# Optimization experiments

Measured on AMD Instinct MI355X. Metric: run time of the kernel, lower is better.

## Reference

```python
import jax, jax.numpy as jnp
import numpy as np

B, N, K = 2, 8192, 16          # batch, points, ED_nsample
SA_C, DG_C = 128, 1024         # SA_conv_out, DG_conv_out
CAT_C = SA_C + SA_C // 4 + 4   # 164 channels into head


def _conv1(W, b, x):
    # 1x1 Conv1d: W [out,in], x [B,in,N]
    return jnp.einsum('oc,bcn->bon', W, x) + b[None, :, None]


def _bn_relu(x, g, be):
    # BatchNorm1d (training-mode batch stats) + ReLU, x [B,C,N]
    m = x.mean(axis=(0, 2), keepdims=True)
    v = x.var(axis=(0, 2), keepdims=True)
    return jax.nn.relu((x - m) * jax.lax.rsqrt(v + 1e-5) * g[None, :, None] + be[None, :, None])


def setup_inputs() -> dict:
    key = jax.random.key(0)
    ks = jax.random.split(key, 32)
    w = lambda k, s: jax.random.normal(k, s, jnp.float32) * 0.05
    p = {}
    p['pointcloud'] = jax.random.normal(ks[0], (B, N, 3), jnp.float32)
    p['h1'] = jax.random.normal(ks[1], (B, SA_C, N), jnp.float32)
    p['h2'] = jax.random.normal(ks[2], (B, DG_C, N), jnp.float32)
    p['numpoints'] = N
    # DG head convs 1024->256->64->32
    p['DG_w1'], p['DG_b1'] = w(ks[3], (256, DG_C)), jnp.zeros(256, jnp.float32)
    p['DG_g1'], p['DG_be1'] = jnp.ones(256, jnp.float32), jnp.zeros(256, jnp.float32)
    p['DG_w2'], p['DG_b2'] = w(ks[4], (64, 256)), jnp.zeros(64, jnp.float32)
    p['DG_g2'], p['DG_be2'] = jnp.ones(64, jnp.float32), jnp.zeros(64, jnp.float32)
    p['DG_w3'], p['DG_b3'] = w(ks[5], (SA_C // 4, 64)), jnp.zeros(SA_C // 4, jnp.float32)
    p['DG_g3'], p['DG_be3'] = jnp.ones(SA_C // 4, jnp.float32), jnp.zeros(SA_C // 4, jnp.float32)
    # ED MLP 3->4->4
    p['ED_w1'], p['ED_b1'] = w(ks[6], (3, 4)), jnp.zeros(4, jnp.float32)
    p['ED_w2'], p['ED_b2'] = w(ks[7], (4, 4)), jnp.zeros(4, jnp.float32)
    # head convs 164->512->256->128
    p['C_w1'], p['C_b1'] = w(ks[8], (512, CAT_C)), jnp.zeros(512, jnp.float32)
    p['C_g1'], p['C_be1'] = jnp.ones(512, jnp.float32), jnp.zeros(512, jnp.float32)
    p['C_w2'], p['C_b2'] = w(ks[9], (256, 512)), jnp.zeros(256, jnp.float32)
    p['C_g2'], p['C_be2'] = jnp.ones(256, jnp.float32), jnp.zeros(256, jnp.float32)
    p['C_w3'], p['C_b3'] = w(ks[10], (128, 256)), jnp.zeros(128, jnp.float32)
    p['C_g3'], p['C_be3'] = jnp.ones(128, jnp.float32), jnp.zeros(128, jnp.float32)
    return p


def reference(pointcloud, h1, h2, numpoints,
              DG_w1, DG_b1, DG_g1, DG_be1, DG_w2, DG_b2, DG_g2, DG_be2,
              DG_w3, DG_b3, DG_g3, DG_be3,
              ED_w1, ED_b1, ED_w2, ED_b2,
              C_w1, C_b1, C_g1, C_be1, C_w2, C_b2, C_g2, C_be2,
              C_w3, C_b3, C_g3, C_be3):
    xyz = pointcloud[..., :3]
    # DG branch head
    h2p = _bn_relu(_conv1(DG_w1, DG_b1, h2), DG_g1, DG_be1)
    h2p = _bn_relu(_conv1(DG_w2, DG_b2, h2p), DG_g2, DG_be2)
    h2p = _bn_relu(_conv1(DG_w3, DG_b3, h2p), DG_g3, DG_be3)
    # ED branch: brute-force knn on squared distances
    sq = jnp.sum(xyz * xyz, axis=-1)                               # [B,N]
    d = sq[:, :, None] + sq[:, None, :] - 2.0 * jnp.einsum('bnd,bmd->bnm', xyz, xyz)
    _, idx = jax.lax.top_k(-d, K)                                  # [B,N,K]
    nbr = jax.vmap(lambda pts, i: pts[i])(xyz, idx)                # [B,N,K,3]
    c = nbr - nbr.mean(axis=2, keepdims=True)
    cov = jnp.einsum('bnkd,bnke->bnde', c, c) / K                  # [B,N,3,3]
    ev = jnp.linalg.eigvalsh(cov)                                  # [B,N,3] ascending
    h3 = jax.nn.relu(ev @ ED_w1 + ED_b1) @ ED_w2 + ED_b2           # [B,N,4]
    # fuse and head
    z = jnp.concatenate([h1, h2p, jnp.transpose(h3, (0, 2, 1))], axis=1)
    z = _bn_relu(_conv1(C_w1, C_b1, z), C_g1, C_be1)
    z = _bn_relu(_conv1(C_w2, C_b2, z), C_g2, C_be2)
    z = _bn_relu(_conv1(C_w3, C_b3, z), C_g3, C_be3)
    return xyz, z
```

## Files before the change

kernel.cpp:

```cpp
#include <hip/hip_runtime.h>

#define NPTS 8192
#define BATCH 2

typedef __attribute__((ext_vector_type(8))) __bf16 bf16x8;
typedef __attribute__((ext_vector_type(4))) float f32x4;
typedef unsigned int u32;

__device__ inline unsigned short f2bf(float x) {
    unsigned u = __float_as_uint(x);
    u += 0x7fffu + ((u >> 16) & 1u);
    return (unsigned short)(u >> 16);
}
__device__ inline unsigned pack32(float d, unsigned idx) {
    unsigned u = __float_as_uint(d);
    u ^= ((unsigned)((int)u >> 31)) | 0x80000000u;
    return (u & 0xFFFFE000u) | idx;
}
__device__ inline unsigned bitonic64u(unsigned key, int lane) {
#pragma unroll
    for (int k = 2; k <= 64; k <<= 1) {
#pragma unroll
        for (int j = k >> 1; j > 0; j >>= 1) {
            unsigned o = __shfl_xor(key, j, 64);
            bool tmin = (((lane & k) == 0) == ((lane & j) == 0));
            key = ((o < key) == tmin) ? o : key;
        }
    }
    return key;
}
__device__ inline void ins16(unsigned& key, unsigned c, int lane) {
    unsigned prev = __shfl_up(key, 1, 64);
    if (lane == 0) prev = 0u;
    unsigned mx = prev > c ? prev : c;
    key = mx < key ? mx : key;
}
__device__ inline float distf(float4 q, float4 p) {
    return fmaf(-2.f, fmaf(q.z, p.z, fmaf(q.y, p.y, q.x * p.x)), q.w + p.w);
}

__global__ __launch_bounds__(256) void prep_presplit(
    const float* __restrict__ pc, float* __restrict__ oxyz, float4* __restrict__ pq,
    const float* __restrict__ W0, const float* __restrict__ W1,
    const float* __restrict__ W2, const float* __restrict__ W3,
    const float* __restrict__ W4, const float* __restrict__ W5,
    unsigned short* __restrict__ wsp) {
    int bx = blockIdx.x, tid = threadIdx.x;
    if (bx < 64) {
        int t = bx * 256 + tid;
        float x = pc[t * 3 + 0], y = pc[t * 3 + 1], z = pc[t * 3 + 2];
        oxyz[t * 3 + 0] = x; oxyz[t * 3 + 1] = y; oxyz[t * 3 + 2] = z;
        pq[t] = make_float4(x, y, z, fmaf(z, z, fmaf(y, y, x * x)));
        return;
    }
    int pb = bx - 64;
    const float* W; int O, C, OP; size_t off; int base;
    if (pb < 1024)      { W = W0; O = 256; C = 1024; OP = 256; off = 0;       base = 0; }
    else if (pb < 1152) { W = W1; O =  64; C =  256; OP = 128; off = 524288;  base = 1024; }
    else if (pb < 1184) { W = W2; O =  32; C =   64; OP = 128; off = 589824;  base = 1152; }
    else if (pb < 1568) { W = W3; O = 512; C =  164; OP = 512; off = 606208;  base = 1184; }
    else if (pb < 2080) { W = W4; O = 256; C =  512; OP = 256; off = 802816;  base = 1568; }
    else                { W = W5; O = 128; C =  256; OP = 128; off = 1064960; base = 2080; }
    unsigned short* dst = wsp + off;
    int t = (pb - base) * 256 + tid;
    int kk = t & 31;
    int o = (t >> 5) % OP;
    int kt = t / (OP * 32);
    int c = kt * 32 + kk;
    float x = (o < O && c < C) ? W[o * C + c] : 0.f;
    unsigned short hb = f2bf(x);
    float hf = __uint_as_float((unsigned)hb << 16);
    unsigned short lb = f2bf(x - hf);
    int s = kk >> 3, pos = kk & 7;
    int sst = s ^ ((o >> 1) & 3);
    dst[((size_t)(kt * 2) * OP + o) * 32 + sst * 8 + pos] = hb;
    dst[((size_t)(kt * 2 + 1) * OP + o) * 32 + sst * 8 + pos] = lb;
}

template <int MODE>
__device__ __forceinline__ void gemm_body(
    int nblk, int oy, int b,
    const unsigned short* __restrict__ Wsp, const float* __restrict__ bias,
    const float* __restrict__ X, float* __restrict__ out,
    int O, int C, int OP, int nK,
    const float2* __restrict__ stats,
    const float* __restrict__ h1, const float* __restrict__ h3,
    const float2* __restrict__ stats3,
    float2* __restrict__ partout) {
    const int N = NPTS;
    int tid = threadIdx.x;
    int lane = tid & 63, w = tid >> 6;
    int wm = w >> 1, wn = w & 1;
    int n0 = nblk * 64, o0 = oy * 64;
    int n = n0 + lane;

    __shared__ __align__(16) unsigned char lds[18432];
    __shared__ float ps1[2][64], ps2[2][64];
    unsigned char* WHp = lds;
    unsigned char* WLp = lds + 4096;
    unsigned char* XHp = lds + 8192;
    unsigned char* XLp = lds + 13312;

    f32x4 acc[2][2];
#pragma unroll
    for (int i = 0; i < 2; ++i)
#pragma unroll
        for (int j = 0; j < 2; ++j) acc[i][j] = (f32x4){0.f, 0.f, 0.f, 0.f};

    float xcur[8], xnxt[8];
    auto loadx = [&](int kt, float (&dst)[8]) {
#pragma unroll
        for (int i = 0; i < 8; ++i) {
            int c = kt * 32 + w * 8 + i;
            float x = 0.f;
            if (MODE == 0 || MODE == 1) {
                if (c < C) x = X[((size_t)(b * C + c)) * N + n];
            } else {
                if (c < 128)       x = h1[((size_t)(b * 128 + c)) * N + n];
                else if (c < 160)  x = X[((size_t)(b * 32 + (c - 128))) * N + n];
                else if (c < 164)  x = h3[((size_t)(b * 4 + (c - 160))) * N + n];
            }
            dst[i] = x;
        }
    };

    loadx(0, xcur);
    for (int kt = 0; kt < nK; ++kt) {
        int c0 = kt * 32;
#pragma unroll
        for (int comp = 0; comp < 2; ++comp) {
            const unsigned short* gb = Wsp + ((size_t)(kt * 2 + comp) * OP + o0) * 32;
            unsigned char* lb = comp ? WLp : WHp;
            __builtin_amdgcn_global_load_lds(
                (const __attribute__((address_space(1))) u32*)(gb + w * 512 + lane * 8),
                (__attribute__((address_space(3))) u32*)(lb + w * 1024),
                16, 0, 0);
        }
        {
            union { bf16x8 s; unsigned short u[8]; } hh, ll;
#pragma unroll
            for (int i = 0; i < 8; ++i) {
                int c = c0 + w * 8 + i;
                float x = xcur[i];
                if (MODE == 1) {
                    if (c < C) {
                        float2 st = stats[c];
                        x = fmaxf(fmaf(x, st.x, st.y), 0.f);
                    }
                } else if (MODE == 2) {
                    if (c >= 128 && c < 160) {
                        float2 st = stats3[c - 128];
                        x = fmaxf(fmaf(x, st.x, st.y), 0.f);
                    }
                }
                unsigned short hb = f2bf(x);
                float hf = __uint_as_float((unsigned)hb << 16);
                unsigned short lb = f2bf(x - hf);
                hh.u[i] = hb; ll.u[i] = lb;
            }
            *(bf16x8*)(XHp + lane * 80 + w * 16) = hh.s;
            *(bf16x8*)(XLp + lane * 80 + w * 16) = ll.s;
        }
        if (kt + 1 < nK) loadx(kt + 1, xnxt);
        __syncthreads();
        {
            int koff = (lane >> 4) * 16;
            bf16x8 bh[2], bl[2];
#pragma unroll
            for (int ni = 0; ni < 2; ++ni) {
                int rb = wn * 32 + ni * 16 + (lane & 15);
                bh[ni] = *(const bf16x8*)(XHp + rb * 80 + koff);
                bl[ni] = *(const bf16x8*)(XLp + rb * 80 + koff);
            }
#pragma unroll
            for (int mi = 0; mi < 2; ++mi) {
                int ra = wm * 32 + mi * 16 + (lane & 15);
                int sw = koff ^ ((((unsigned)ra >> 1) & 3) * 16);
                bf16x8 ah = *(const bf16x8*)(WHp + ra * 64 + sw);
                bf16x8 al = *(const bf16x8*)(WLp + ra * 64 + sw);
#pragma unroll
                for (int ni = 0; ni < 2; ++ni) {
                    acc[mi][ni] = __builtin_amdgcn_mfma_f32_16x16x32_bf16(ah, bh[ni], acc[mi][ni], 0, 0, 0);
                    acc[mi][ni] = __builtin_amdgcn_mfma_f32_16x16x32_bf16(ah, bl[ni], acc[mi][ni], 0, 0, 0);
                    acc[mi][ni] = __builtin_amdgcn_mfma_f32_16x16x32_bf16(al, bh[ni], acc[mi][ni], 0, 0, 0);
                }
            }
        }
        __syncthreads();
        if (kt + 1 < nK) {
#pragma unroll
            for (int i = 0; i < 8; ++i) xcur[i] = xnxt[i];
        }
    }
    int col = lane & 15, rq = lane >> 4;
#pragma unroll
    for (int mi = 0; mi < 2; ++mi) {
#pragma unroll
        for (int j = 0; j < 4; ++j) {
            int oloc = wm * 32 + mi * 16 + rq * 4 + j;
            int o = o0 + oloc;
            float s1 = 0.f, s2 = 0.f;
            if (o < O) {
                float bs = bias[o];
                float v0 = acc[mi][0][j] + bs;
                float v1 = acc[mi][1][j] + bs;
                float* po = out + ((size_t)(b * O + o)) * N + n0 + wn * 32 + col;
                po[0] = v0; po[16] = v1;
                s1 = v0 + v1;
                s2 = fmaf(v0, v0, v1 * v1);
            }
#pragma unroll
            for (int mm = 1; mm < 16; mm <<= 1) {
                s1 += __shfl_xor(s1, mm, 64);
                s2 += __shfl_xor(s2, mm, 64);
            }
            if (col == 0) { ps1[wn][oloc] = s1; ps2[wn][oloc] = s2; }
        }
    }
    __syncthreads();
    if (tid < 64) {
        int o = o0 + tid;
        if (o < O)
            partout[(size_t)o * 256 + b * 128 + nblk] =
                make_float2(ps1[0][tid] + ps1[1][tid], ps2[0][tid] + ps2[1][tid]);
    }
}

template <int MODE>
__global__ __launch_bounds__(256, 4) void mfma_gemm(
    const unsigned short* __restrict__ Wsp, const float* __restrict__ bias,
    const float* __restrict__ X, float* __restrict__ out,
    int O, int C, int OP, int nK,
    const float2* __restrict__ stats,
    const float* __restrict__ h1, const float* __restrict__ h3,
    const float2* __restrict__ stats3,
    float2* __restrict__ partout) {
    gemm_body<MODE>(blockIdx.x, blockIdx.y, blockIdx.z, Wsp, bias, X, out, O, C, OP, nK,
                    stats, h1, h3, stats3, partout);
}

__device__ void knn_body(int kb, const float4* __restrict__ pq,
                         const float* __restrict__ ew1, const float* __restrict__ eb1,
                         const float* __restrict__ ew2, const float* __restrict__ eb2,
                         float* __restrict__ h3) {
    int wv = threadIdx.x >> 6;
    int lane = threadIdx.x & 63;
    int sg = kb * 4 + wv;
    int b = sg >> 12;
    int iloc = (sg & 4095) << 1;
    const float4* pqb = pq + (size_t)b * NPTS;
    float4 Q0 = pqb[iloc + 0], Q1 = pqb[iloc + 1];

    float4 p = pqb[lane];
    unsigned k0 = bitonic64u(pack32(distf(Q0, p), lane), lane);
    unsigned k1 = bitonic64u(pack32(distf(Q1, p), lane), lane);
    unsigned tk0 = (unsigned)__builtin_amdgcn_readlane((int)k0, 15);
    unsigned tk1 = (unsigned)__builtin_amdgcn_readlane((int)k1, 15);

    float4 A = pqb[64 + lane];
    float4 B = pqb[128 + lane];
    for (int it = 1; it + 1 < 128; it += 2) {
        int tbA = it * 64, tbB = tbA + 64;
        int t3 = (it + 3 < 128) ? it + 3 : 0;
        float4 Cx = pqb[(it + 2) * 64 + lane];
        float4 Dx = pqb[t3 * 64 + lane];
        unsigned cA0 = pack32(distf(Q0, A), tbA + lane);
        unsigned cA1 = pack32(distf(Q1, A), tbA + lane);
        unsigned cB0 = pack32(distf(Q0, B), tbB + lane);
        unsigned cB1 = pack32(distf(Q1, B), tbB + lane);
        unsigned long long mA0 = __ballot(cA0 < tk0), mB0 = __ballot(cB0 < tk0);
        unsigned long long mA1 = __ballot(cA1 < tk1), mB1 = __ballot(cB1 < tk1);
        if (mA0 | mA1 | mB0 | mB1) {
            while (mA0) {
                int L = __ffsll((long long)mA0) - 1; mA0 &= mA0 - 1;
                ins16(k0, (unsigned)__builtin_amdgcn_readlane((int)cA0, L), lane);
            }
            while (mB0) {
                int L = __ffsll((long long)mB0) - 1; mB0 &= mB0 - 1;
                ins16(k0, (unsigned)__builtin_amdgcn_readlane((int)cB0, L), lane);
            }
            while (mA1) {
                int L = __ffsll((long long)mA1) - 1; mA1 &= mA1 - 1;
                ins16(k1, (unsigned)__builtin_amdgcn_readlane((int)cA1, L), lane);
            }
            while (mB1) {
                int L = __ffsll((long long)mB1) - 1; mB1 &= mB1 - 1;
                ins16(k1, (unsigned)__builtin_amdgcn_readlane((int)cB1, L), lane);
            }
            tk0 = (unsigned)__builtin_amdgcn_readlane((int)k0, 15);
            tk1 = (unsigned)__builtin_amdgcn_readlane((int)k1, 15);
        }
        A = Cx; B = Dx;
    }
    {
        int tbA = 127 * 64;
        unsigned cA0 = pack32(distf(Q0, A), tbA + lane);
        unsigned cA1 = pack32(distf(Q1, A), tbA + lane);
        unsigned long long mA0 = __ballot(cA0 < tk0);
        unsigned long long mA1 = __ballot(cA1 < tk1);
        while (mA0) {
            int L = __ffsll((long long)mA0) - 1; mA0 &= mA0 - 1;
            ins16(k0, (unsigned)__builtin_amdgcn_readlane((int)cA0, L), lane);
        }
        while (mA1) {
            int L = __ffsll((long long)mA1) - 1; mA1 &= mA1 - 1;
            ins16(k1, (unsigned)__builtin_amdgcn_readlane((int)cA1, L), lane);
        }
    }

    int g = lane >> 4, r = lane & 15;
    unsigned j0 = ((unsigned)__shfl((int)k0, r, 64)) & 8191u;
    unsigned j1 = ((unsigned)__shfl((int)k1, r, 64)) & 8191u;
    unsigned nj = ((g & 1) == 0) ? j0 : j1;

    float4 nb = pqb[nj];
    float sx = nb.x, sy = nb.y, sz = nb.z;
#pragma unroll
    for (int m = 1; m < 16; m <<= 1) {
        sx += __shfl_xor(sx, m, 64);
        sy += __shfl_xor(sy, m, 64);
        sz += __shfl_xor(sz, m, 64);
    }
    const float i16 = 1.f / 16.f;
    float cx = nb.x - sx * i16, cy = nb.y - sy * i16, cz = nb.z - sz * i16;
    float xx = cx * cx, xy = cx * cy, xz = cx * cz, yy = cy * cy, yz = cy * cz, zz = cz * cz;
#pragma unroll
    for (int m = 1; m < 16; m <<= 1) {
        xx += __shfl_xor(xx, m, 64); xy += __shfl_xor(xy, m, 64); xz += __shfl_xor(xz, m, 64);
        yy += __shfl_xor(yy, m, 64); yz += __shfl_xor(yz, m, 64); zz += __shfl_xor(zz, m, 64);
    }
    float a11 = xx * i16, a12 = xy * i16, a13 = xz * i16,
          a22 = yy * i16, a23 = yz * i16, a33 = zz * i16;
    float q = (a11 + a22 + a33) * (1.f / 3.f);
    float p1 = a12 * a12 + a13 * a13 + a23 * a23;
    float b11 = a11 - q, b22 = a22 - q, b33 = a33 - q;
    float p2 = b11 * b11 + b22 * b22 + b33 * b33 + 2.f * p1;
    float pr = sqrtf(p2 * (1.f / 6.f));
    float ipv = (p2 > 1e-32f) ? (1.f / pr) : 0.f;
    float detB = b11 * (b22 * b33 - a23 * a23) - a12 * (a12 * b33 - a23 * a13) +
                 a13 * (a12 * a23 - b22 * a13);
    float r3 = 0.5f * detB * ipv * ipv * ipv;
    r3 = fminf(1.f, fmaxf(-1.f, r3));
    float phi = acosf(r3) * (1.f / 3.f);
    float e1 = q + 2.f * pr * cosf(phi);
    float e3 = q + 2.f * pr * cosf(phi + 2.0943951023931953f);
    float e2 = 3.f * q - e1 - e3;
    float ev0 = e3, ev1 = e2, ev2 = e1;
    float h[4], o[4];
#pragma unroll
    for (int kk = 0; kk < 4; ++kk)
        h[kk] = fmaxf(eb1[kk] + ev0 * ew1[kk] + ev1 * ew1[4 + kk] + ev2 * ew1[8 + kk], 0.f);
#pragma unroll
    for (int kk = 0; kk < 4; ++kk)
        o[kk] = eb2[kk] + h[0] * ew2[kk] + h[1] * ew2[4 + kk] + h[2] * ew2[8 + kk] +
                h[3] * ew2[12 + kk];
    int ipt = iloc + (g & 1);
    if (r == 0 && g < 2) {
#pragma unroll
        for (int kk = 0; kk < 4; ++kk) h3[(b * 4 + kk) * NPTS + ipt] = o[kk];
    }
}

__global__ __launch_bounds__(256, 4) void dg1_knn(
    const unsigned short* __restrict__ Wsp, const float* __restrict__ bias,
    const float* __restrict__ X, float* __restrict__ out, float2* __restrict__ partout,
    const float4* __restrict__ pq,
    const float* __restrict__ ew1, const float* __restrict__ eb1,
    const float* __restrict__ ew2, const float* __restrict__ eb2,
    float* __restrict__ h3) {
    if (blockIdx.x < 1024) {
        int bid = blockIdx.x;
        gemm_body<0>(bid & 127, (bid >> 7) & 3, bid >> 9, Wsp, bias, X, out,
                     256, 1024, 256, 32, nullptr, nullptr, nullptr, nullptr, partout);
    } else {
        knn_body(blockIdx.x - 1024, pq, ew1, eb1, ew2, eb2, h3);
    }
}

__global__ __launch_bounds__(256) void finalize_kernel(const float2* __restrict__ part,
                                                       const float* __restrict__ g,
                                                       const float* __restrict__ be,
                                                       float2* __restrict__ st) {
    int c = blockIdx.x;
    int tid = threadIdx.x;
    __shared__ float r1[256], r2[256];
    float2 v = part[(size_t)c * 256 + tid];
    r1[tid] = v.x; r2[tid] = v.y;
    __syncthreads();
    for (int off = 128; off > 0; off >>= 1) {
        if (tid < off) { r1[tid] += r1[tid + off]; r2[tid] += r2[tid + off]; }
        __syncthreads();
    }
    if (tid == 0) {
        const float inv = 1.f / (BATCH * NPTS);
        float m = r1[0] * inv;
        float var = r2[0] * inv - m * m;
        float sc = g[c] * rsqrtf(var + 1e-5f);
        st[c] = make_float2(sc, be[c] - m * sc);
    }
}

__global__ __launch_bounds__(256) void stats_final_kernel(
    const float2* __restrict__ part, const float* __restrict__ g,
    const float* __restrict__ be, const float* __restrict__ X,
    float* __restrict__ outz) {
    const int N = NPTS;
    const int C = 128;
    int c = blockIdx.x;
    int tid = threadIdx.x;
    __shared__ float r1[256], r2[256];
    __shared__ float2 stv;
    float2 v = part[(size_t)c * 256 + tid];
    r1[tid] = v.x; r2[tid] = v.y;
    __syncthreads();
    for (int off = 128; off > 0; off >>= 1) {
        if (tid < off) { r1[tid] += r1[tid + off]; r2[tid] += r2[tid + off]; }
        __syncthreads();
    }
    if (tid == 0) {
        const float inv = 1.f / (BATCH * NPTS);
        float m = r1[0] * inv;
        float var = r2[0] * inv - m * m;
        float sc = g[c] * rsqrtf(var + 1e-5f);
        stv = make_float2(sc, be[c] - m * sc);
    }
    __syncthreads();
    float2 s = stv;
    for (int b = 0; b < BATCH; ++b) {
        const float* p = X + (size_t)(b * C + c) * N;
        float* q = outz + (size_t)(b * C + c) * N;
        for (int nn = tid * 4; nn < N; nn += 1024) {
            float4 v4 = *(const float4*)(p + nn);
            v4.x = fmaxf(fmaf(v4.x, s.x, s.y), 0.f);
            v4.y = fmaxf(fmaf(v4.y, s.x, s.y), 0.f);
            v4.z = fmaxf(fmaf(v4.z, s.x, s.y), 0.f);
            v4.w = fmaxf(fmaf(v4.w, s.x, s.y), 0.f);
            *(float4*)(q + nn) = v4;
        }
    }
}

extern "C" void kernel_launch(void* const* d_in, const int* in_sizes, int n_in,
                              void* d_out, int out_size, void* d_ws, size_t ws_size,
                              hipStream_t stream) {
    const float* pc    = (const float*)d_in[0];
    const float* h1    = (const float*)d_in[1];
    const float* h2    = (const float*)d_in[2];
    const float* DG_w1 = (const float*)d_in[4];
    const float* DG_b1 = (const float*)d_in[5];
    const float* DG_g1 = (const float*)d_in[6];
    const float* DG_be1= (const float*)d_in[7];
    const float* DG_w2 = (const float*)d_in[8];
    const float* DG_b2 = (const float*)d_in[9];
    const float* DG_g2 = (const float*)d_in[10];
    const float* DG_be2= (const float*)d_in[11];
    const float* DG_w3 = (const float*)d_in[12];
    const float* DG_b3 = (const float*)d_in[13];
    const float* DG_g3 = (const float*)d_in[14];
    const float* DG_be3= (const float*)d_in[15];
    const float* ED_w1 = (const float*)d_in[16];
    const float* ED_b1 = (const float*)d_in[17];
    const float* ED_w2 = (const float*)d_in[18];
    const float* ED_b2 = (const float*)d_in[19];
    const float* C_w1  = (const float*)d_in[20];
    const float* C_b1  = (const float*)d_in[21];
    const float* C_g1  = (const float*)d_in[22];
    const float* C_be1 = (const float*)d_in[23];
    const float* C_w2  = (const float*)d_in[24];
    const float* C_b2  = (const float*)d_in[25];
    const float* C_g2  = (const float*)d_in[26];
    const float* C_be2 = (const float*)d_in[27];
    const float* C_w3  = (const float*)d_in[28];
    const float* C_b3  = (const float*)d_in[29];
    const float* C_g3  = (const float*)d_in[30];
    const float* C_be3 = (const float*)d_in[31];

    float* ws = (float*)d_ws;
    float* A  = ws;
    float* Bb = ws + (8l << 20);
    float* Cc = ws + (12l << 20);
    float* H3 = ws + (14l << 20);
    float4* PQ = (float4*)(H3 + 65536);
    float2* ST = (float2*)(H3 + 131072);
    unsigned short* WSP = (unsigned short*)(H3 + 131072 + 2560);

    float2* P_DG1 = (float2*)(Bb + (1l << 20));
    float2* P_DG2 = (float2*)(Bb + (1l << 20) + 131072);
    float2* P_DG3 = (float2*)(Bb + (1l << 20) + 131072 + 32768);
    float2* P_C1  = (float2*)(Cc + (1l << 20));
    float2* TAIL  = (float2*)(WSP + 1130496);
    float2* P_C2  = TAIL;
    float2* P_C3  = TAIL + 65536;

    const size_t W1SP = 0;
    const size_t W2SP = 524288;
    const size_t W3SP = 589824;
    const size_t C1SP = 606208;
    const size_t C2SP = 802816;
    const size_t C3SP = 1064960;

    float* outxyz = (float*)d_out;
    float* outz   = (float*)d_out + BATCH * NPTS * 3;

    prep_presplit<<<2272, 256, 0, stream>>>(pc, outxyz, PQ,
                                            DG_w1, DG_w2, DG_w3, C_w1, C_w2, C_w3, WSP);

    dg1_knn<<<3072, 256, 0, stream>>>(WSP + W1SP, DG_b1, h2, A, P_DG1,
                                      PQ, ED_w1, ED_b1, ED_w2, ED_b2, H3);
    finalize_kernel<<<256, 256, 0, stream>>>(P_DG1, DG_g1, DG_be1, ST + 0);
    mfma_gemm<1><<<dim3(128, 1, 2), 256, 0, stream>>>(WSP + W2SP, DG_b2, A, Bb, 64, 256, 128, 8,
                                                      ST + 0, nullptr, nullptr, nullptr, P_DG2);
    finalize_kernel<<<64, 256, 0, stream>>>(P_DG2, DG_g2, DG_be2, ST + 256);
    mfma_gemm<1><<<dim3(128, 1, 2), 256, 0, stream>>>(WSP + W3SP, DG_b3, Bb, Cc, 32, 64, 128, 2,
                                                      ST + 256, nullptr, nullptr, nullptr, P_DG3);
    finalize_kernel<<<32, 256, 0, stream>>>(P_DG3, DG_g3, DG_be3, ST + 320);

    mfma_gemm<2><<<dim3(128, 8, 2), 256, 0, stream>>>(WSP + C1SP, C_b1, Cc, A, 512, 164, 512, 6,
                                                      nullptr, h1, H3, ST + 320, P_C1);
    finalize_kernel<<<512, 256, 0, stream>>>(P_C1, C_g1, C_be1, ST + 352);
    mfma_gemm<1><<<dim3(128, 4, 2), 256, 0, stream>>>(WSP + C2SP, C_b2, A, Bb, 256, 512, 256, 16,
                                                      ST + 352, nullptr, nullptr, nullptr, P_C2);
    finalize_kernel<<<256, 256, 0, stream>>>(P_C2, C_g2, C_be2, ST + 864);
    mfma_gemm<1><<<dim3(128, 2, 2), 256, 0, stream>>>(WSP + C3SP, C_b3, Bb, Cc, 128, 256, 128, 8,
                                                      ST + 864, nullptr, nullptr, nullptr, P_C3);

    stats_final_kernel<<<128, 256, 0, stream>>>(P_C3, C_g3, C_be3, Cc, outz);
}
```

Before: 263.3 us.

## Move head-weight presplit into the dg1/knn kernel and prioritize knn waves

Measured after the change: 265.7 us. No clear change (+0.9%).

```diff
diff --git a/kernel.cpp b/kernel.cpp
--- a/kernel.cpp
+++ b/kernel.cpp
@@ -38,31 +38,8 @@
 __device__ inline float distf(float4 q, float4 p) {
     return fmaf(-2.f, fmaf(q.z, p.z, fmaf(q.y, p.y, q.x * p.x)), q.w + p.w);
 }
-
-__global__ __launch_bounds__(256) void prep_presplit(
-    const float* __restrict__ pc, float* __restrict__ oxyz, float4* __restrict__ pq,
-    const float* __restrict__ W0, const float* __restrict__ W1,
-    const float* __restrict__ W2, const float* __restrict__ W3,
-    const float* __restrict__ W4, const float* __restrict__ W5,
-    unsigned short* __restrict__ wsp) {
-    int bx = blockIdx.x, tid = threadIdx.x;
-    if (bx < 64) {
-        int t = bx * 256 + tid;
-        float x = pc[t * 3 + 0], y = pc[t * 3 + 1], z = pc[t * 3 + 2];
-        oxyz[t * 3 + 0] = x; oxyz[t * 3 + 1] = y; oxyz[t * 3 + 2] = z;
-        pq[t] = make_float4(x, y, z, fmaf(z, z, fmaf(y, y, x * x)));
-        return;
-    }
-    int pb = bx - 64;
-    const float* W; int O, C, OP; size_t off; int base;
-    if (pb < 1024)      { W = W0; O = 256; C = 1024; OP = 256; off = 0;       base = 0; }
-    else if (pb < 1152) { W = W1; O =  64; C =  256; OP = 128; off = 524288;  base = 1024; }
-    else if (pb < 1184) { W = W2; O =  32; C =   64; OP = 128; off = 589824;  base = 1152; }
-    else if (pb < 1568) { W = W3; O = 512; C =  164; OP = 512; off = 606208;  base = 1184; }
-    else if (pb < 2080) { W = W4; O = 256; C =  512; OP = 256; off = 802816;  base = 1568; }
-    else                { W = W5; O = 128; C =  256; OP = 128; off = 1064960; base = 2080; }
-    unsigned short* dst = wsp + off;
-    int t = (pb - base) * 256 + tid;
+__device__ inline void presplit_body(const float* __restrict__ W, int O, int C, int OP,
+                                     unsigned short* __restrict__ dst, int t) {
     int kk = t & 31;
     int o = (t >> 5) % OP;
     int kt = t / (OP * 32);
@@ -75,6 +52,25 @@
     int sst = s ^ ((o >> 1) & 3);
     dst[((size_t)(kt * 2) * OP + o) * 32 + sst * 8 + pos] = hb;
     dst[((size_t)(kt * 2 + 1) * OP + o) * 32 + sst * 8 + pos] = lb;
+}
+
+__global__ __launch_bounds__(256) void prep_presplit(
+    const float* __restrict__ pc, float* __restrict__ oxyz, float4* __restrict__ pq,
+    const float* __restrict__ W0, const float* __restrict__ W1,
+    const float* __restrict__ W2,
+    unsigned short* __restrict__ wsp) {
+    int bx = blockIdx.x, tid = threadIdx.x;
+    if (bx < 64) {
+        int t = bx * 256 + tid;
+        float x = pc[t * 3 + 0], y = pc[t * 3 + 1], z = pc[t * 3 + 2];
+        oxyz[t * 3 + 0] = x; oxyz[t * 3 + 1] = y; oxyz[t * 3 + 2] = z;
+        pq[t] = make_float4(x, y, z, fmaf(z, z, fmaf(y, y, x * x)));
+        return;
+    }
+    int pb = bx - 64;
+    if (pb < 1024)      presplit_body(W0, 256, 1024, 256, wsp + 0,      pb * 256 + tid);
+    else if (pb < 1152) presplit_body(W1,  64,  256, 128, wsp + 524288, (pb - 1024) * 256 + tid);
+    else                presplit_body(W2,  32,   64, 128, wsp + 589824, (pb - 1152) * 256 + tid);
 }
 
 template <int MODE>
@@ -367,13 +363,23 @@
     const float4* __restrict__ pq,
     const float* __restrict__ ew1, const float* __restrict__ eb1,
     const float* __restrict__ ew2, const float* __restrict__ eb2,
-    float* __restrict__ h3) {
+    float* __restrict__ h3,
+    const float* __restrict__ W3, const float* __restrict__ W4,
+    const float* __restrict__ W5, unsigned short* __restrict__ wsp) {
     if (blockIdx.x < 1024) {
         int bid = blockIdx.x;
         gemm_body<0>(bid & 127, (bid >> 7) & 3, bid >> 9, Wsp, bias, X, out,
                      256, 1024, 256, 32, nullptr, nullptr, nullptr, nullptr, partout);
+    } else if (blockIdx.x < 3072) {
+        __builtin_amdgcn_s_setprio(1);
+        knn_body(blockIdx.x - 1024, pq, ew1, eb1, ew2, eb2, h3);
+        __builtin_amdgcn_s_setprio(0);
     } else {
-        knn_body(blockIdx.x - 1024, pq, ew1, eb1, ew2, eb2, h3);
+        int pb = blockIdx.x - 3072;
+        int tid = threadIdx.x;
+        if (pb < 384)      presplit_body(W3, 512, 164, 512, wsp + 606208,  pb * 256 + tid);
+        else if (pb < 896) presplit_body(W4, 256, 512, 256, wsp + 802816,  (pb - 384) * 256 + tid);
+        else               presplit_body(W5, 128, 256, 128, wsp + 1064960, (pb - 896) * 256 + tid);
     }
 }
 
@@ -502,11 +508,11 @@
     float* outxyz = (float*)d_out;
     float* outz   = (float*)d_out + BATCH * NPTS * 3;
 
-    prep_presplit<<<2272, 256, 0, stream>>>(pc, outxyz, PQ,
-                                            DG_w1, DG_w2, DG_w3, C_w1, C_w2, C_w3, WSP);
-
-    dg1_knn<<<3072, 256, 0, stream>>>(WSP + W1SP, DG_b1, h2, A, P_DG1,
-                                      PQ, ED_w1, ED_b1, ED_w2, ED_b2, H3);
+    prep_presplit<<<1248, 256, 0, stream>>>(pc, outxyz, PQ, DG_w1, DG_w2, DG_w3, WSP);
+
+    dg1_knn<<<4096, 256, 0, stream>>>(WSP + W1SP, DG_b1, h2, A, P_DG1,
+                                      PQ, ED_w1, ED_b1, ED_w2, ED_b2, H3,
+                                      C_w1, C_w2, C_w3, WSP);
     finalize_kernel<<<256, 256, 0, stream>>>(P_DG1, DG_g1, DG_be1, ST + 0);
     mfma_gemm<1><<<dim3(128, 1, 2), 256, 0, stream>>>(WSP + W2SP, DG_b2, A, Bb, 64, 256, 128, 8,
                                                       ST + 0, nullptr, nullptr, nullptr, P_DG2);
```
